# Performance work log

Hardware: AMD Instinct MI355X
Metric: run time of the kernel (lower is better)

Reference implementation:

```python
import jax, jax.numpy as jnp
import numpy as np

D_STATE = 48
D_CONV = 4
DT_RANK = 12
SEG = 4  # path=3 -> segment=2**(3-1)
EPS = 1e-5


def _layernorm(x, w, b):
    m = x.mean(-1, keepdims=True)
    v = x.var(-1, keepdims=True)
    return (x - m) / jnp.sqrt(v + EPS) * w + b


def _batchnorm(x, g, b):
    # x: (B, N, C); BatchNorm1d in train mode normalizes per channel over (B, N)
    m = x.mean(axis=(0, 1))
    v = x.var(axis=(0, 1))
    return (x - m) / jnp.sqrt(v + EPS) * g + b


def _selective_scan(u, delta, A, Bm, Cm):
    # u, delta: (b,l,d); A: (d,n); Bm, Cm: (b,l,n)
    def step(h, inp):
        dt_t, b_t, c_t, u_t = inp  # (b,d),(b,n),(b,n),(b,d)
        dA = jnp.exp(dt_t[:, :, None] * A)                  # (b,d,n)
        h = dA * h + (dt_t * u_t)[:, :, None] * b_t[:, None, :]
        y = jnp.einsum('bdn,bn->bd', h, c_t)
        return h, y
    b, l, d = u.shape
    n = A.shape[1]
    h0 = jnp.zeros((b, d, n), u.dtype)
    xs = (delta.transpose(1, 0, 2), Bm.transpose(1, 0, 2),
          Cm.transpose(1, 0, 2), u.transpose(1, 0, 2))
    _, ys = jax.lax.scan(step, h0, xs)
    return ys.transpose(1, 0, 2)


def _mamba(x, in_proj_w, conv_w, conv_b, x_proj_w, dt_proj_w, dt_proj_b,
           A_log, D_param, out_proj_w):
    b, l, _ = x.shape
    xz = x @ in_proj_w.T                                   # (b,l,2*di)
    xa, z = jnp.split(xz, 2, axis=-1)
    # causal depthwise conv1d, kernel D_CONV, left pad D_CONV-1
    xp = jnp.pad(xa, ((0, 0), (D_CONV - 1, 0), (0, 0)))
    xc = sum(xp[:, k:k + l, :] * conv_w[:, k] for k in range(D_CONV)) + conv_b
    xc = jax.nn.silu(xc)
    x_dbl = xc @ x_proj_w.T                                # (b,l,dt_rank+2n)
    dtl = x_dbl[..., :DT_RANK]
    Bm = x_dbl[..., DT_RANK:DT_RANK + D_STATE]
    Cm = x_dbl[..., DT_RANK + D_STATE:]
    dt = jax.nn.softplus(dtl @ dt_proj_w.T + dt_proj_b)
    A = -jnp.exp(A_log)
    y = _selective_scan(xc, dt, A, Bm, Cm) + xc * D_param
    y = y * jax.nn.silu(z)
    return y @ out_proj_w.T


def _ffn(x, fc1_w, bn1_g, bn1_b, r_w, i_w, rb, ib, fc2_w, bn2_g, bn2_b):
    h = jax.nn.relu(_batchnorm(x @ fc1_w.T, bn1_g, bn1_b))
    hf = jnp.fft.fft(h, axis=1, norm='ortho')
    # torch.einsum('bnc,cc->bnc', X, W) takes diag(W): elementwise channel scale
    rd = jnp.diagonal(r_w)
    idg = jnp.diagonal(i_w)
    real = jax.nn.relu(hf.real * rd - hf.imag * idg + rb)
    imag = jax.nn.relu(hf.imag * rd + hf.real * idg + ib)
    xt = jnp.fft.ifft(jax.lax.complex(real, imag), axis=1, norm='ortho').real
    return _batchnorm(xt @ fc2_w.T, bn2_g, bn2_b)


def _block(x, in_proj_w, conv_w, conv_b, x_proj_w, dt_proj_w, dt_proj_b,
           A_log, D_param, out_proj_w, mnorm_w, mnorm_b,
           norm1_w, norm1_b, norm2_w, norm2_b,
           fc1_w, bn1_g, bn1_b, r_w, i_w, rb, ib, fc2_w, bn2_g, bn2_b):
    B, D, C = x.shape
    tt = D // SEG
    # multi-path shifted copies: first D - i*tt positions shifted by i*tt,
    # tail keeps the original values (clone semantics)
    shifts = [x] + [jnp.concatenate([x[:, i * tt:], x[:, D - i * tt:]], axis=1)
                    for i in range(1, SEG)]
    xo = jnp.concatenate(shifts, axis=0)                   # (SEG*B, D, C)
    y = _mamba(_layernorm(xo, mnorm_w, mnorm_b),
               in_proj_w, conv_w, conv_b, x_proj_w, dt_proj_w, dt_proj_b,
               A_log, D_param, out_proj_w)
    ys = y.reshape(SEG, B, D, C)
    segs = [ys[0][:, :tt]]
    for i in range(1, SEG):
        s = ys[0][:, tt * i:tt * (i + 1)]
        for j in range(i):
            s = s + ys[j + 1][:, tt * (i - j - 1):tt * (i - j)]
        segs.append(s / (i + 1))
    xo0 = jnp.concatenate(segs, axis=1)                    # (B, D, C)
    x1 = x + _layernorm(xo0, norm1_w, norm1_b)
    x2 = x1 + _ffn(_layernorm(x1, norm2_w, norm2_b),
                   fc1_w, bn1_g, bn1_b, r_w, i_w, rb, ib, fc2_w, bn2_g, bn2_b)
    return x2


def setup_inputs() -> dict:
    key = jax.random.key(0)
    ks = jax.random.split(key, 16)
    s = 0.02
    B, L, C = 8, 512, 192
    DI, HD = 384, 384  # d_inner = 2*dim, ffn hidden = mlp_ratio*dim
    rn = lambda k, shp: jax.random.normal(k, shp, dtype=jnp.float32)
    return dict(
        x=rn(ks[0], (B, L, C)),
        in_proj_w=s * rn(ks[1], (2 * DI, C)),
        conv_w=s * rn(ks[2], (DI, D_CONV)),
        conv_b=s * rn(ks[3], (DI,)),
        x_proj_w=s * rn(ks[4], (DT_RANK + 2 * D_STATE, DI)),
        dt_proj_w=s * rn(ks[5], (DI, DT_RANK)),
        dt_proj_b=s * rn(ks[6], (DI,)),
        A_log=jnp.log(jnp.tile(jnp.arange(1, D_STATE + 1, dtype=jnp.float32), (DI, 1))),
        D_param=jnp.ones((DI,), jnp.float32),
        out_proj_w=s * rn(ks[7], (C, DI)),
        mnorm_w=jnp.ones((C,), jnp.float32), mnorm_b=jnp.zeros((C,), jnp.float32),
        norm1_w=jnp.ones((C,), jnp.float32), norm1_b=jnp.zeros((C,), jnp.float32),
        norm2_w=jnp.ones((C,), jnp.float32), norm2_b=jnp.zeros((C,), jnp.float32),
        fc1_w=s * rn(ks[8], (HD, C)),
        bn1_g=jnp.ones((HD,), jnp.float32), bn1_b=jnp.zeros((HD,), jnp.float32),
        r_w=s * rn(ks[9], (HD, HD)),
        i_w=s * rn(ks[10], (HD, HD)),
        rb=s * rn(ks[11], (HD,)),
        ib=s * rn(ks[12], (HD,)),
        fc2_w=s * rn(ks[13], (C, HD)),
        bn2_g=jnp.ones((C,), jnp.float32), bn2_b=jnp.zeros((C,), jnp.float32),
    )


def reference(x, in_proj_w, conv_w, conv_b, x_proj_w, dt_proj_w, dt_proj_b,
              A_log, D_param, out_proj_w, mnorm_w, mnorm_b,
              norm1_w, norm1_b, norm2_w, norm2_b,
              fc1_w, bn1_g, bn1_b, r_w, i_w, rb, ib, fc2_w, bn2_g, bn2_b):
    return _block(x, in_proj_w, conv_w, conv_b, x_proj_w, dt_proj_w, dt_proj_b,
                  A_log, D_param, out_proj_w, mnorm_w, mnorm_b,
                  norm1_w, norm1_b, norm2_w, norm2_b,
                  fc1_w, bn1_g, bn1_b, r_w, i_w, rb, ib, fc2_w, bn2_g, bn2_b)
```

## Files before the change

### kernel.cpp

```cpp
#include <hip/hip_runtime.h>
#include <math.h>

#define LSEQ 512
#define CDIM 192
#define DIN  384
#define NST  48
#define RNK  12
#define NBT  32
#define NB   8
#define NCH  16
#define LCH  32

static __device__ __forceinline__ float sigmoidf_(float x) { return 1.f / (1.f + __expf(-x)); }

typedef __attribute__((ext_vector_type(8))) short bshort8;
typedef __attribute__((ext_vector_type(4))) float f32x4;

static __device__ __forceinline__ short f2bf(float x) {
    unsigned u = __float_as_uint(x);
    unsigned r = (u + 0x7FFFu + ((u >> 16) & 1u)) >> 16;
    return (short)r;
}
static __device__ __forceinline__ float bfhi2f(unsigned pk) { return __uint_as_float(pk & 0xffff0000u); }
static __device__ __forceinline__ float bflo2f(unsigned pk) { return __uint_as_float(pk << 16); }

#define SP 40
template<int BM, int BN, int GATE>
__global__ __launch_bounds__(256) void gemm_mfma_kernel(
    const float* __restrict__ A, const float* __restrict__ B, float* __restrict__ C,
    int M, int N, int K, int lda, int ldb, int ldc,
    long long sA, long long sB_, long long sC_,
    int transB, int accsub,
    const float* __restrict__ gxc, const float* __restrict__ gxz, const float* __restrict__ gD)
{
    constexpr int WM = BM / 2, WN = BN / 2, MI = WM / 16, NI = WN / 16;
    __shared__ short As[BM * SP];
    __shared__ short Bs[BN * SP];
    int tid = threadIdx.x;
    int m0 = blockIdx.x * BM, n0 = blockIdx.y * BN;
    if (GATE) {
        int sseg = m0 >> 12, t0 = m0 & 511;
        if ((t0 >> 7) + sseg > 3) return;
    }
    A += (long long)blockIdx.z * sA;
    B += (long long)blockIdx.z * sB_;
    C += (long long)blockIdx.z * sC_;
    int lane = tid & 63, wid = tid >> 6;
    int wr = wid >> 1, wc = wid & 1;
    int lr = lane & 15, lg = lane >> 4;
    f32x4 acc[MI][NI] = {};

    for (int k0 = 0; k0 < K; k0 += 32) {
#pragma unroll
        for (int it = 0; it < BM * 8 / 256; ++it) {
            int idx = tid + it * 256;
            int row = idx >> 3, kq = idx & 7;
            long long gm = m0 + row;
            float4 v = *(const float4*)(A + gm * lda + k0 + kq * 4);
            if (GATE) {
                int sseg = (int)(gm >> 12), bb = (int)((gm >> 9) & 7), tt = (int)(gm & 511);
                long long src = (long long)bb * 512 + tt + 128 * sseg;
                float4 xcv = *(const float4*)(gxc + src * 384 + k0 + kq * 4);
                float4 zv  = *(const float4*)(gxz + src * 768 + 384 + k0 + kq * 4);
                float4 Dv  = *(const float4*)(gD + k0 + kq * 4);
                v.x = (v.x + xcv.x * Dv.x) * (zv.x * sigmoidf_(zv.x));
                v.y = (v.y + xcv.y * Dv.y) * (zv.y * sigmoidf_(zv.y));
                v.z = (v.z + xcv.z * Dv.z) * (zv.z * sigmoidf_(zv.z));
                v.w = (v.w + xcv.w * Dv.w) * (zv.w * sigmoidf_(zv.w));
            }
            short4 b4 = make_short4(f2bf(v.x), f2bf(v.y), f2bf(v.z), f2bf(v.w));
            *(short4*)(&As[row * SP + kq * 4]) = b4;
        }
        if (transB) {
#pragma unroll
            for (int it = 0; it < BN * 8 / 256; ++it) {
                int idx = tid + it * 256;
                int row = idx >> 3, kq = idx & 7;
                int gn = n0 + row;
                float4 v = make_float4(0.f, 0.f, 0.f, 0.f);
                if (gn < N) v = *(const float4*)(B + (long long)gn * ldb + k0 + kq * 4);
                short4 b4 = make_short4(f2bf(v.x), f2bf(v.y), f2bf(v.z), f2bf(v.w));
                *(short4*)(&Bs[row * SP + kq * 4]) = b4;
            }
        } else {
            constexpr int NQ = BN / 4;
#pragma unroll
            for (int it = 0; it < 32 * NQ / 256; ++it) {
                int idx = tid + it * 256;
                int k = idx / NQ, nq = idx % NQ;
                int gn = n0 + nq * 4;
                float4 v = make_float4(0.f, 0.f, 0.f, 0.f);
                if (gn < N) v = *(const float4*)(B + (long long)(k0 + k) * ldb + gn);
                Bs[(nq * 4 + 0) * SP + k] = f2bf(v.x);
                Bs[(nq * 4 + 1) * SP + k] = f2bf(v.y);
                Bs[(nq * 4 + 2) * SP + k] = f2bf(v.z);
                Bs[(nq * 4 + 3) * SP + k] = f2bf(v.w);
            }
        }
        __syncthreads();
        bshort8 af[MI], bfr[NI];
#pragma unroll
        for (int i = 0; i < MI; ++i)
            af[i] = *(const bshort8*)(&As[(wr * WM + i * 16 + lr) * SP + lg * 8]);
#pragma unroll
        for (int j = 0; j < NI; ++j)
            bfr[j] = *(const bshort8*)(&Bs[(wc * WN + j * 16 + lr) * SP + lg * 8]);
#pragma unroll
        for (int i = 0; i < MI; ++i)
#pragma unroll
            for (int j = 0; j < NI; ++j)
                acc[i][j] = __builtin_amdgcn_mfma_f32_16x16x32_bf16(af[i], bfr[j], acc[i][j], 0, 0, 0);
        __syncthreads();
    }
#pragma unroll
    for (int i = 0; i < MI; ++i) {
        int gm = m0 + wr * WM + i * 16 + lg * 4;
#pragma unroll
        for (int j = 0; j < NI; ++j) {
            int gn = n0 + wc * WN + j * 16 + lr;
            if (gn < N) {
#pragma unroll
                for (int r = 0; r < 4; ++r) {
                    long long idx = (long long)(gm + r) * ldc + gn;
                    float v = acc[i][j][r];
                    if (accsub) C[idx] = C[idx] - v;
                    else C[idx] = v;
                }
            }
        }
    }
}

__global__ __launch_bounds__(256) void dft_fwd_kernel(
    const short* __restrict__ Tc, const short* __restrict__ Ts,
    const float* __restrict__ Bm, float* __restrict__ C1, float* __restrict__ C2,
    const float* __restrict__ stats, const float* __restrict__ bng,
    const float* __restrict__ bnb, float invM)
{
    __shared__ short Acs[64 * SP];
    __shared__ short Ass[64 * SP];
    __shared__ short Bs[64 * SP];
    int tid = threadIdx.x;
    int m0 = blockIdx.x * 64, n0 = blockIdx.y * 64;
    const float* B = Bm + (long long)blockIdx.z * 196608;
    float* c1 = C1 + (long long)blockIdx.z * 122880;
    float* c2 = C2 + (long long)blockIdx.z * 122880;
    int lane = tid & 63, wid = tid >> 6;
    int wr = wid >> 1, wc = wid & 1;
    int lr = lane & 15, lg = lane >> 4;
    int nn = tid & 63, k8 = tid >> 6;
    int f = n0 + nn;
    float sc, sh;
    {
        float m = stats[f] * invM;
        float vv = stats[384 + f] * invM - m * m;
        sc = rsqrtf(vv + 1e-5f) * bng[f];
        sh = bnb[f] - m * sc;
    }
    f32x4 a1[2][2] = {}, a2[2][2] = {};
    for (int k0 = 0; k0 < 512; k0 += 32) {
        {
            *(uint4*)(&Acs[nn * SP + k8 * 8]) =
                *(const uint4*)(Tc + (long long)(m0 + nn) * 512 + k0 + k8 * 8);
            *(uint4*)(&Ass[nn * SP + k8 * 8]) =
                *(const uint4*)(Ts + (long long)(m0 + nn) * 512 + k0 + k8 * 8);
        }
        {
            bshort8 pk;
#pragma unroll
            for (int j = 0; j < 8; ++j) {
                float v = B[(long long)(k0 + k8 * 8 + j) * 384 + f];
                v = fmaxf(fmaf(v, sc, sh), 0.f);
                pk[j] = f2bf(v);
            }
            *(bshort8*)(&Bs[nn * SP + k8 * 8]) = pk;
        }
        __syncthreads();
        bshort8 af[2], sf[2], bf[2];
#pragma unroll
        for (int i = 0; i < 2; ++i) {
            af[i] = *(const bshort8*)(&Acs[(wr * 32 + i * 16 + lr) * SP + lg * 8]);
            sf[i] = *(const bshort8*)(&Ass[(wr * 32 + i * 16 + lr) * SP + lg * 8]);
            bf[i] = *(const bshort8*)(&Bs[(wc * 32 + i * 16 + lr) * SP + lg * 8]);
        }
#pragma unroll
        for (int i = 0; i < 2; ++i)
#pragma unroll
            for (int j = 0; j < 2; ++j) {
                a1[i][j] = __builtin_amdgcn_mfma_f32_16x16x32_bf16(af[i], bf[j], a1[i][j], 0, 0, 0);
                a2[i][j] = __builtin_amdgcn_mfma_f32_16x16x32_bf16(sf[i], bf[j], a2[i][j], 0, 0, 0);
            }
        __syncthreads();
    }
#pragma unroll
    for (int i = 0; i < 2; ++i) {
        int gm = m0 + wr * 32 + i * 16 + lg * 4;
#pragma unroll
        for (int j = 0; j < 2; ++j) {
            int gn = n0 + wc * 32 + j * 16 + lr;
#pragma unroll
            for (int r = 0; r < 4; ++r) {
                c1[(long long)(gm + r) * 384 + gn] = a1[i][j][r];
                c2[(long long)(gm + r) * 384 + gn] = a2[i][j][r];
            }
        }
    }
}

__global__ __launch_bounds__(256) void dft_inv_kernel(
    const short* __restrict__ Tc, const short* __restrict__ Ts,
    const float* __restrict__ Br, const float* __restrict__ Bi,
    float* __restrict__ Co,
    const float* __restrict__ rw, const float* __restrict__ iw,
    const float* __restrict__ rbv, const float* __restrict__ ibv)
{
    __shared__ short Acs[64 * SP];
    __shared__ short Ans[64 * SP];
    __shared__ short Brs[64 * SP];
    __shared__ short Bis[64 * SP];
    int tid = threadIdx.x;
    int m0 = blockIdx.x * 64, n0 = blockIdx.y * 64;
    const float* br = Br + (long long)blockIdx.z * 122880;
    const float* bi = Bi + (long long)blockIdx.z * 122880;
    float* co = Co + (long long)blockIdx.z * 196608;
    int lane = tid & 63, wid = tid >> 6;
    int wr = wid >> 1, wc = wid & 1;
    int lr = lane & 15, lg = lane >> 4;
    int nn = tid & 63, k8 = tid >> 6;
    int f = n0 + nn;
    float rd = rw[(long long)f * 384 + f];
    float id = iw[(long long)f * 384 + f];
    float rbs = rbv[f], ibs = ibv[f];
    f32x4 acc[2][2] = {};
    for (int k0 = 0; k0 < 288; k0 += 32) {
        {
            *(uint4*)(&Acs[nn * SP + k8 * 8]) =
                *(const uint4*)(Tc + (long long)(m0 + nn) * 512 + k0 + k8 * 8);
            uint4 ps = *(const uint4*)(Ts + (long long)(m0 + nn) * 512 + k0 + k8 * 8);
            ps.x ^= 0x80008000u; ps.y ^= 0x80008000u; ps.z ^= 0x80008000u; ps.w ^= 0x80008000u;
            *(uint4*)(&Ans[nn * SP + k8 * 8]) = ps;
        }
        {
            bshort8 pr, pi;
#pragma unroll
            for (int j = 0; j < 8; ++j) {
                int kg = k0 + k8 * 8 + j;
                short vr = 0, vi = 0;
                if (kg <= 256) {
                    float Re = br[(long long)kg * 384 + f];
                    float S  = bi[(long long)kg * 384 + f];
                    float wgt = (kg == 0 || kg == 256) ? 0.5f : 1.f;
                    float t1 = Re * rd + rbs, t2 = S * id;
                    float t3 = Re * id + ibs, t4 = S * rd;
                    float Rs = wgt * (fmaxf(t1 + t2, 0.f) + fmaxf(t1 - t2, 0.f));
                    float Is = wgt * (fmaxf(t3 - t4, 0.f) - fmaxf(t3 + t4, 0.f));
                    vr = f2bf(Rs);
                    vi = f2bf(Is);
                }
                pr[j] = vr;
                pi[j] = vi;
            }
            *(bshort8*)(&Brs[nn * SP + k8 * 8]) = pr;
            *(bshort8*)(&Bis[nn * SP + k8 * 8]) = pi;
        }
        __syncthreads();
        bshort8 af[2], nf[2], rf[2], iff[2];
#pragma unroll
        for (int i = 0; i < 2; ++i) {
            af[i]  = *(const bshort8*)(&Acs[(wr * 32 + i * 16 + lr) * SP + lg * 8]);
            nf[i]  = *(const bshort8*)(&Ans[(wr * 32 + i * 16 + lr) * SP + lg * 8]);
            rf[i]  = *(const bshort8*)(&Brs[(wc * 32 + i * 16 + lr) * SP + lg * 8]);
            iff[i] = *(const bshort8*)(&Bis[(wc * 32 + i * 16 + lr) * SP + lg * 8]);
        }
#pragma unroll
        for (int i = 0; i < 2; ++i)
#pragma unroll
            for (int j = 0; j < 2; ++j) {
                acc[i][j] = __builtin_amdgcn_mfma_f32_16x16x32_bf16(af[i], rf[j], acc[i][j], 0, 0, 0);
                acc[i][j] = __builtin_amdgcn_mfma_f32_16x16x32_bf16(nf[i], iff[j], acc[i][j], 0, 0, 0);
            }
        __syncthreads();
    }
#pragma unroll
    for (int i = 0; i < 2; ++i) {
        int gm = m0 + wr * 32 + i * 16 + lg * 4;
#pragma unroll
        for (int j = 0; j < 2; ++j) {
            int gn = n0 + wc * 32 + j * 16 + lr;
#pragma unroll
            for (int r = 0; r < 4; ++r)
                co[(long long)(gm + r) * 384 + gn] = acc[i][j][r];
        }
    }
}

__global__ __launch_bounds__(64) void ln_kernel(
    const float* __restrict__ in, const float* __restrict__ w, const float* __restrict__ b,
    float* __restrict__ out)
{
    int row = blockIdx.x;
    const float* xr = in + (long long)row * CDIM;
    int lane = threadIdx.x;
    float v0 = xr[lane], v1 = xr[lane + 64], v2 = xr[lane + 128];
    float s1 = v0 + v1 + v2;
    float s2 = v0 * v0 + v1 * v1 + v2 * v2;
#pragma unroll
    for (int off = 32; off >= 1; off >>= 1) {
        s1 += __shfl_xor(s1, off);
        s2 += __shfl_xor(s2, off);
    }
    float mean = s1 * (1.f / 192.f);
    float var = s2 * (1.f / 192.f) - mean * mean;
    float rstd = rsqrtf(var + 1e-5f);
    float* orow = out + (long long)row * CDIM;
    orow[lane]       = (v0 - mean) * rstd * w[lane] + b[lane];
    orow[lane + 64]  = (v1 - mean) * rstd * w[lane + 64] + b[lane + 64];
    orow[lane + 128] = (v2 - mean) * rstd * w[lane + 128] + b[lane + 128];
}

__global__ __launch_bounds__(256) void conv_silu_kernel(
    const float* __restrict__ xz, const float* __restrict__ cw,
    const float* __restrict__ cb, float* __restrict__ xc)
{
    long long idx = (long long)blockIdx.x * 256 + threadIdx.x;
    int d = (int)(idx % DIN);
    long long rt = idx / DIN;
    int t = (int)(rt & 511);
    long long base = rt - t;
    float acc = cb[d];
#pragma unroll
    for (int k = 0; k < 4; ++k) {
        int tt = t + k - 3;
        if (tt >= 0) acc = fmaf(xz[(base + tt) * 768 + d], cw[d * 4 + k], acc);
    }
    xc[idx] = acc * sigmoidf_(acc);
}

__global__ __launch_bounds__(256) void scan_pass1(
    const float* __restrict__ xdbl0, const float* __restrict__ xc0,
    const float* __restrict__ dt_w, const float* __restrict__ dt_b,
    const float* __restrict__ A_log, float* __restrict__ ylocal,
    float* __restrict__ hpart, float* __restrict__ sumdt, float* __restrict__ cumdtg)
{
    int d0 = blockIdx.x * 32, bb = blockIdx.y, c = blockIdx.z;
    __shared__ float sBC[LCH][96];
    __shared__ unsigned sdd[LCH][32];
    __shared__ float sdtl[LCH][12];
    __shared__ float sdtw[32][12];
    __shared__ float sdtb[32];
    int tid = threadIdx.x;
    int p = tid >> 3, q = tid & 7, d = d0 + p;
    for (int i = tid; i < 384; i += 256) sdtw[i / 12][i % 12] = dt_w[(d0 + i / 12) * 12 + i % 12];
    if (tid < 32) sdtb[tid] = dt_b[d0 + tid];
    float A0 = -__expf(A_log[d * NST + 6 * q]);
    float Ad = -__expf(A_log[d * NST + 6 * q + 1]) - A0;
    long long srcbase = (long long)bb * LSEQ + c * LCH;
    for (int i = tid; i < LCH * 108; i += 256) {
        int tt = i / 108, cc = i % 108;
        float v = xdbl0[(srcbase + tt) * 108 + cc];
        if (cc < 12) sdtl[tt][cc] = v;
        else if (cc < 60) { int n = cc - 12; int qq = (n * 43) >> 8; sBC[tt][qq * 12 + (n - qq * 6)] = v; }
        else              { int n = cc - 60; int qq = (n * 43) >> 8; sBC[tt][qq * 12 + 6 + (n - qq * 6)] = v; }
    }
    __syncthreads();
    for (int i = tid; i < LCH * 32; i += 256) {
        int tt = i >> 5, j = i & 31;
        float s = sdtb[j];
#pragma unroll
        for (int r = 0; r < 12; ++r) s = fmaf(sdtl[tt][r], sdtw[j][r], s);
        s = fmaxf(s, 0.f) + log1pf(__expf(-fabsf(s)));
        float u = xc0[(srcbase + tt) * DIN + d0 + j];
        unsigned hi = (unsigned)(unsigned short)f2bf(s);
        unsigned lo = (unsigned)(unsigned short)f2bf(s * u);
        sdd[tt][j] = (hi << 16) | lo;
    }
    __syncthreads();
    float h0r = 0.f, h1r = 0.f, h2r = 0.f, h3r = 0.f, h4r = 0.f, h5r = 0.f;
    float cum = 0.f;
    long long locbase = ((long long)(bb * NCH + c)) * LCH;
#pragma unroll 2
    for (int tt = 0; tt < LCH; ++tt) {
        unsigned pk = sdd[tt][p];
        float s = bfhi2f(pk), du = bflo2f(pk);
        cum += s;
        float f = __expf(s * A0);
        float w = __expf(s * Ad);
        float4 v0 = *(const float4*)&sBC[tt][q * 12];
        float4 v1 = *(const float4*)&sBC[tt][q * 12 + 4];
        float4 v2 = *(const float4*)&sBC[tt][q * 12 + 8];
        float y;
        h0r = fmaf(f, h0r, du * v0.x); y = h0r * v1.z;          f *= w;
        h1r = fmaf(f, h1r, du * v0.y); y = fmaf(h1r, v1.w, y);  f *= w;
        h2r = fmaf(f, h2r, du * v0.z); y = fmaf(h2r, v2.x, y);  f *= w;
        h3r = fmaf(f, h3r, du * v0.w); y = fmaf(h3r, v2.y, y);  f *= w;
        h4r = fmaf(f, h4r, du * v1.x); y = fmaf(h4r, v2.z, y);  f *= w;
        h5r = fmaf(f, h5r, du * v1.y); y = fmaf(h5r, v2.w, y);
        y += __shfl_xor(y, 1);
        y += __shfl_xor(y, 2);
        y += __shfl_xor(y, 4);
        if (q == 0) {
            ylocal[(locbase + tt) * DIN + d] = y;
            cumdtg[(srcbase + tt) * DIN + d] = cum;
        }
    }
    if (q == 0) sumdt[((long long)(bb * NCH + c)) * DIN + d] = cum;
    float* hp = &hpart[(((long long)(bb * NCH + c)) * DIN + d) * NST + 6 * q];
    hp[0] = h0r; hp[1] = h1r; hp[2] = h2r; hp[3] = h3r; hp[4] = h4r; hp[5] = h5r;
}

__global__ __launch_bounds__(256) void scan_pass2(
    const float* __restrict__ A_log, const float* __restrict__ sumdt,
    const float* __restrict__ hpart, float* __restrict__ hinbuf)
{
    long long idx = (long long)blockIdx.x * 256 + threadIdx.x;
    if (idx >= 8LL * DIN * NST) return;
    int n = (int)(idx % NST);
    long long rem = idx / NST;
    int d = (int)(rem % DIN);
    int bb = (int)(rem / DIN);
    float An = -__expf(A_log[d * NST + n]);
    float S[NCH], P[NCH];
#pragma unroll
    for (int c = 0; c < NCH; ++c) {
        S[c] = hpart[(((long long)(bb * NCH + c)) * DIN + d) * NST + n];
        P[c] = __expf(An * sumdt[((long long)(bb * NCH + c)) * DIN + d]);
    }
#pragma unroll
    for (int s = 0; s < 4; ++s) {
        float hin = 0.f;
#pragma unroll
        for (int c = 0; c < NCH; ++c) {
            if (c < 4 * s) continue;
            int ch = c - 4 * s;
            hinbuf[(((long long)(bb * 64 + s * 16 + ch)) * DIN + d) * NST + n] = hin;
            hin = fmaf(P[c], hin, S[c]);
        }
    }
}

#define TT3 16
__global__ __launch_bounds__(256) void scan_pass3(
    const float* __restrict__ xdbl0, const float* __restrict__ cumdtg,
    const float* __restrict__ A_log, const float* __restrict__ hin_g,
    const float* __restrict__ ylocal, float* __restrict__ yout)
{
    int c = blockIdx.z >> 1, tq = blockIdx.z & 1;
    int toff = tq * TT3;
    int d0 = blockIdx.x * 32, bb = blockIdx.y;
    int smax = (c >> 2) < 3 ? (c >> 2) : 3;
    __shared__ float sC[TT3][64];
    __shared__ float scum[TT3][32];
    int tid = threadIdx.x;
    int p = tid >> 3, q = tid & 7, d = d0 + p;
    float A0 = -__expf(A_log[d * NST + 6 * q]);
    float Ad = -__expf(A_log[d * NST + 6 * q + 1]) - A0;
    float g0[6] = {}, g1[6] = {}, g2[6] = {}, g3[6] = {};
    {
        const float* hp0 = &hin_g[(((long long)(bb * 64 + 0 * 16 + c)) * DIN + d) * NST + 6 * q];
#pragma unroll
        for (int k = 0; k < 6; ++k) g0[k] = hp0[k];
        if (smax >= 1) {
            const float* hp1 = &hin_g[(((long long)(bb * 64 + 1 * 16 + (c - 4))) * DIN + d) * NST + 6 * q];
#pragma unroll
            for (int k = 0; k < 6; ++k) g1[k] = hp1[k];
        }
        if (smax >= 2) {
            const float* hp2 = &hin_g[(((long long)(bb * 64 + 2 * 16 + (c - 8))) * DIN + d) * NST + 6 * q];
#pragma unroll
            for (int k = 0; k < 6; ++k) g2[k] = hp2[k];
        }
        if (smax >= 3) {
            const float* hp3 = &hin_g[(((long long)(bb * 64 + 3 * 16 + (c - 12))) * DIN + d) * NST + 6 * q];
#pragma unroll
            for (int k = 0; k < 6; ++k) g3[k] = hp3[k];
        }
    }
    long long srcbase = (long long)bb * LSEQ + c * LCH + toff;
    long long locbase = ((long long)(bb * NCH + c)) * LCH + toff;
    long long ob0 = ((long long)(0 * NB + bb)) * LSEQ + (long long)c * LCH + toff;
    long long ob1 = ((long long)(1 * NB + bb)) * LSEQ + (long long)(c - 4) * LCH + toff;
    long long ob2 = ((long long)(2 * NB + bb)) * LSEQ + (long long)(c - 8) * LCH + toff;
    long long ob3 = ((long long)(3 * NB + bb)) * LSEQ + (long long)(c - 12) * LCH + toff;
    for (int i = tid; i < TT3 * 48; i += 256) {
        int tt = i / 48, n = i % 48;
        int qq = (n * 43) >> 8;
        sC[tt][qq * 8 + n - qq * 6] = xdbl0[(srcbase + tt) * 108 + 60 + n];
    }
    for (int i = tid; i < TT3 * 32; i += 256) {
        int tt = i >> 5, j = i & 31;
        scum[tt][j] = cumdtg[(srcbase + tt) * DIN + d0 + j];
    }
    __syncthreads();
#pragma unroll 2
    for (int tt = 0; tt < TT3; ++tt) {
        float cd = scum[tt][p];
        float f = __expf(cd * A0);
        float w = __expf(cd * Ad);
        float4 c03 = *(const float4*)&sC[tt][q * 8];
        float4 c45 = *(const float4*)&sC[tt][q * 8 + 4];
        float Cf0 = c03.x * f; f *= w;
        float Cf1 = c03.y * f; f *= w;
        float Cf2 = c03.z * f; f *= w;
        float Cf3 = c03.w * f; f *= w;
        float Cf4 = c45.x * f; f *= w;
        float Cf5 = c45.y * f;
        float a0 = Cf0 * g0[0];
        a0 = fmaf(Cf1, g0[1], a0); a0 = fmaf(Cf2, g0[2], a0);
        a0 = fmaf(Cf3, g0[3], a0); a0 = fmaf(Cf4, g0[4], a0);
        a0 = fmaf(Cf5, g0[5], a0);
        a0 += __shfl_xor(a0, 1); a0 += __shfl_xor(a0, 2); a0 += __shfl_xor(a0, 4);
        float a1 = 0.f, a2 = 0.f, a3 = 0.f;
        if (smax >= 1) {
            a1 = Cf0 * g1[0];
            a1 = fmaf(Cf1, g1[1], a1); a1 = fmaf(Cf2, g1[2], a1);
            a1 = fmaf(Cf3, g1[3], a1); a1 = fmaf(Cf4, g1[4], a1);
            a1 = fmaf(Cf5, g1[5], a1);
            a1 += __shfl_xor(a1, 1); a1 += __shfl_xor(a1, 2); a1 += __shfl_xor(a1, 4);
        }
        if (smax >= 2) {
            a2 = Cf0 * g2[0];
            a2 = fmaf(Cf1, g2[1], a2); a2 = fmaf(Cf2, g2[2], a2);
            a2 = fmaf(Cf3, g2[3], a2); a2 = fmaf(Cf4, g2[4], a2);
            a2 = fmaf(Cf5, g2[5], a2);
            a2 += __shfl_xor(a2, 1); a2 += __shfl_xor(a2, 2); a2 += __shfl_xor(a2, 4);
        }
        if (smax >= 3) {
            a3 = Cf0 * g3[0];
            a3 = fmaf(Cf1, g3[1], a3); a3 = fmaf(Cf2, g3[2], a3);
            a3 = fmaf(Cf3, g3[3], a3); a3 = fmaf(Cf4, g3[4], a3);
            a3 = fmaf(Cf5, g3[5], a3);
            a3 += __shfl_xor(a3, 1); a3 += __shfl_xor(a3, 2); a3 += __shfl_xor(a3, 4);
        }
        if (q == 0) {
            float yl = ylocal[(locbase + tt) * DIN + d];
            yout[(ob0 + tt) * DIN + d] = yl + a0;
            if (smax >= 1) yout[(ob1 + tt) * DIN + d] = yl + a1;
            if (smax >= 2) yout[(ob2 + tt) * DIN + d] = yl + a2;
            if (smax >= 3) yout[(ob3 + tt) * DIN + d] = yl + a3;
        }
    }
}

__global__ __launch_bounds__(64) void combine_ln_kernel(
    const float* __restrict__ ym, const float* __restrict__ x,
    const float* __restrict__ w, const float* __restrict__ b,
    const float* __restrict__ w2, const float* __restrict__ b2,
    float* __restrict__ x1, float* __restrict__ lnx1)
{
    int row = blockIdx.x;
    int t = row & 511, bb = row >> 9;
    int i = t >> 7;
    int lane = threadIdx.x;
    float vals[3];
#pragma unroll
    for (int cp = 0; cp < 3; ++cp) {
        int c = lane + cp * 64;
        float v = ym[((long long)bb * LSEQ + t) * CDIM + c];
        for (int j = 1; j <= i; ++j)
            v += ym[((long long)(j * NB + bb) * LSEQ + (t - 128 * j)) * CDIM + c];
        vals[cp] = v / (float)(i + 1);
    }
    float s1 = vals[0] + vals[1] + vals[2];
    float s2 = vals[0] * vals[0] + vals[1] * vals[1] + vals[2] * vals[2];
#pragma unroll
    for (int off = 32; off >= 1; off >>= 1) {
        s1 += __shfl_xor(s1, off);
        s2 += __shfl_xor(s2, off);
    }
    float mean = s1 * (1.f / 192.f);
    float var = s2 * (1.f / 192.f) - mean * mean;
    float rstd = rsqrtf(var + 1e-5f);
    long long base = (long long)row * CDIM;
    float xv[3];
#pragma unroll
    for (int cp = 0; cp < 3; ++cp) {
        int c = lane + cp * 64;
        xv[cp] = x[base + c] + (vals[cp] - mean) * rstd * w[c] + b[c];
        x1[base + c] = xv[cp];
    }
    float t1 = xv[0] + xv[1] + xv[2];
    float t2 = xv[0] * xv[0] + xv[1] * xv[1] + xv[2] * xv[2];
#pragma unroll
    for (int off = 32; off >= 1; off >>= 1) {
        t1 += __shfl_xor(t1, off);
        t2 += __shfl_xor(t2, off);
    }
    float mean2 = t1 * (1.f / 192.f);
    float var2 = t2 * (1.f / 192.f) - mean2 * mean2;
    float rstd2 = rsqrtf(var2 + 1e-5f);
#pragma unroll
    for (int cp = 0; cp < 3; ++cp) {
        int c = lane + cp * 64;
        lnx1[base + c] = (xv[cp] - mean2) * rstd2 * w2[c] + b2[c];
    }
}

__global__ __launch_bounds__(256) void bnstats_kernel(
    const float* __restrict__ X, float* __restrict__ stats, int NF)
{
    int fl = threadIdx.x & 63;
    int f = blockIdx.x * 64 + fl;
    int r = threadIdx.x >> 6;
    int t0 = blockIdx.y * 128;
    float s1 = 0.f, s2 = 0.f;
    for (int i = 0; i < 32; ++i) {
        int row = t0 + r * 32 + i;
        float v = X[(long long)row * NF + f];
        s1 += v;
        s2 += v * v;
    }
    __shared__ float p1[4][64], p2[4][64];
    p1[r][fl] = s1;
    p2[r][fl] = s2;
    __syncthreads();
    if (threadIdx.x < 64) {
        int ff = blockIdx.x * 64 + threadIdx.x;
        float a = p1[0][threadIdx.x] + p1[1][threadIdx.x] + p1[2][threadIdx.x] + p1[3][threadIdx.x];
        float c = p2[0][threadIdx.x] + p2[1][threadIdx.x] + p2[2][threadIdx.x] + p2[3][threadIdx.x];
        atomicAdd(&stats[ff], a);
        atomicAdd(&stats[NF + ff], c);
    }
}

__global__ __launch_bounds__(256) void bnapply_kernel(
    const float* __restrict__ X, const float* __restrict__ stats,
    const float* __restrict__ g, const float* __restrict__ b,
    const float* __restrict__ residual, float* __restrict__ out,
    int NF, int relu, float invM)
{
    long long idx = (long long)blockIdx.x * 256 + threadIdx.x;
    int f = (int)(idx % NF);
    float mean = stats[f] * invM;
    float var = stats[NF + f] * invM - mean * mean;
    float v = (X[idx] - mean) * rsqrtf(var + 1e-5f) * g[f] + b[f];
    if (relu) v = fmaxf(v, 0.f);
    if (residual) v += residual[idx];
    out[idx] = v;
}

__global__ __launch_bounds__(256) void dft_table_kernel(short* __restrict__ tc, short* __restrict__ ts)
{
    int idx = blockIdx.x * 256 + threadIdx.x;
    int k = idx >> 9, t = idx & 511;
    int r = (k * t) & 511;
    float th = (float)r * (6.283185307179586f / 512.f);
    float s, c;
    __sincosf(th, &s, &c);
    const float inv = 0.04419417382415922f;
    tc[idx] = f2bf(c * inv);
    ts[idx] = f2bf(s * inv);
}

extern "C" void kernel_launch(void* const* d_in, const int* in_sizes, int n_in,
                              void* d_out, int out_size, void* d_ws, size_t ws_size,
                              hipStream_t stream)
{
    const float* x        = (const float*)d_in[0];
    const float* in_w     = (const float*)d_in[1];
    const float* conv_w   = (const float*)d_in[2];
    const float* conv_b   = (const float*)d_in[3];
    const float* xproj_w  = (const float*)d_in[4];
    const float* dtp_w    = (const float*)d_in[5];
    const float* dtp_b    = (const float*)d_in[6];
    const float* A_log    = (const float*)d_in[7];
    const float* D_par    = (const float*)d_in[8];
    const float* outp_w   = (const float*)d_in[9];
    const float* mnw      = (const float*)d_in[10];
    const float* mnb      = (const float*)d_in[11];
    const float* n1w      = (const float*)d_in[12];
    const float* n1b      = (const float*)d_in[13];
    const float* n2w      = (const float*)d_in[14];
    const float* n2b      = (const float*)d_in[15];
    const float* fc1_w    = (const float*)d_in[16];
    const float* bn1g     = (const float*)d_in[17];
    const float* bn1b     = (const float*)d_in[18];
    const float* r_w      = (const float*)d_in[19];
    const float* i_w      = (const float*)d_in[20];
    const float* rb       = (const float*)d_in[21];
    const float* ib       = (const float*)d_in[22];
    const float* fc2_w    = (const float*)d_in[23];
    const float* bn2g     = (const float*)d_in[24];
    const float* bn2b     = (const float*)d_in[25];
    float* out = (float*)d_out;
    float* ws = (float*)d_ws;

    float* lnx0   = ws;
    float* xz0    = lnx0   + 786432LL;
    float* xc0    = xz0    + 3145728LL;
    float* xdbl0  = xc0    + 1572864LL;
    float* yscan  = xdbl0  + 442368LL;
    float* hinb   = yscan  + 6291456LL;
    float* cumdtg = hinb   + 9437184LL;
    float* hpart  = cumdtg + 1572864LL;
    float* ylocal = hpart  + 2359296LL;
    float* sumdt  = ylocal + 1572864LL;
    float* ymout = hinb;
    float* x1    = lnx0;
    float* lnx1  = yscan;
    float* hbuf  = yscan + 786432LL;
    float* hfr   = yscan + 2359296LL;
    float* hfi   = yscan + 3342336LL;
    float* xt    = xz0;
    float* g0    = xz0 + 1572864LL;
    short* tabc_bf = (short*)xc0;
    short* tabs_bf = (short*)(xc0 + 131072LL);
    float* stats = xc0 + 262144LL;

    ln_kernel<<<dim3(NB * LSEQ), dim3(64), 0, stream>>>(x, mnw, mnb, lnx0);

    gemm_mfma_kernel<64, 128, 0><<<dim3(64, 6, 1), dim3(256), 0, stream>>>(
        lnx0, in_w, xz0, 4096, 768, 192, 192, 192, 768, 0, 0, 0, 1, 0,
        nullptr, nullptr, nullptr);

    conv_silu_kernel<<<dim3(6144), dim3(256), 0, stream>>>(xz0, conv_w, conv_b, xc0);

    gemm_mfma_kernel<64, 64, 0><<<dim3(64, 2, 1), dim3(256), 0, stream>>>(
        xc0, xproj_w, xdbl0, 4096, 108, 384, 384, 384, 108, 0, 0, 0, 1, 0,
        nullptr, nullptr, nullptr);

    scan_pass1<<<dim3(12, 8, NCH), dim3(256), 0, stream>>>(
        xdbl0, xc0, dtp_w, dtp_b, A_log, ylocal, hpart, sumdt, cumdtg);
    scan_pass2<<<dim3(576), dim3(256), 0, stream>>>(A_log, sumdt, hpart, hinb);
    scan_pass3<<<dim3(12, 8, NCH * 2), dim3(256), 0, stream>>>(
        xdbl0, cumdtg, A_log, hinb, ylocal, yscan);

    gemm_mfma_kernel<64, 64, 1><<<dim3(256, 3, 1), dim3(256), 0, stream>>>(
        yscan, outp_w, ymout, 16384, 192, 384, 384, 384, 192, 0, 0, 0, 1, 0,
        xc0, xz0, D_par);

    hipMemsetAsync(stats, 0, 2048 * sizeof(float), stream);

    combine_ln_kernel<<<dim3(NB * LSEQ), dim3(64), 0, stream>>>(
        ymout, x, n1w, n1b, n2w, n2b, x1, lnx1);

    gemm_mfma_kernel<64, 64, 0><<<dim3(64, 6, 1), dim3(256), 0, stream>>>(
        lnx1, fc1_w, hbuf, 4096, 384, 192, 192, 192, 384, 0, 0, 0, 1, 0,
        nullptr, nullptr, nullptr);

    bnstats_kernel<<<dim3(6, 32), dim3(256), 0, stream>>>(hbuf, stats, 384);

    dft_table_kernel<<<dim3(1024), dim3(256), 0, stream>>>(tabc_bf, tabs_bf);

    dft_fwd_kernel<<<dim3(5, 6, 8), dim3(256), 0, stream>>>(
        tabc_bf, tabs_bf, hbuf, hfr, hfi, stats, bn1g, bn1b, 1.f / 4096.f);

    dft_inv_kernel<<<dim3(8, 6, 8), dim3(256), 0, stream>>>(
        tabc_bf, tabs_bf, hfr, hfi, xt, r_w, i_w, rb, ib);

    gemm_mfma_kernel<32, 64, 0><<<dim3(128, 3, 1), dim3(256), 0, stream>>>(
        xt, fc2_w, g0, 4096, 192, 384, 384, 384, 192, 0, 0, 0, 1, 0,
        nullptr, nullptr, nullptr);

    bnstats_kernel<<<dim3(3, 32), dim3(256), 0, stream>>>(g0, stats + 1024, 192);
    bnapply_kernel<<<dim3(3072), dim3(256), 0, stream>>>(
        g0, stats + 1024, bn2g, bn2b, x1, out, 192, 0, 1.f / 4096.f);
}
```

Baseline: 260.4 us.

## Collapse four segment scans into one averaged carried-state scan before out-projection

The four shifted-segment Mamba outputs are now averaged before the out-projection rather than after it. This relies on the linearity of out_proj and of the gating applied to y. scan_pass2 builds a single weighted-average incoming state per chunk (hbar), so scan_pass3 computes one correction instead of up to four and updates ylocal in place. The out-projection GEMM runs on 4096 rows instead of 16384, and combine_ln no longer sums four segment outputs. Workspace aliases are reshuffled to fit the smaller buffers; the in-place ylocal update and the new hfi placement risk aliasing errors.

```diff
diff --git a/kernel.cpp b/kernel.cpp
--- a/kernel.cpp
+++ b/kernel.cpp
@@ -6,7 +6,6 @@
 #define DIN  384
 #define NST  48
 #define RNK  12
-#define NBT  32
 #define NB   8
 #define NCH  16
 #define LCH  32
@@ -38,10 +37,6 @@
     __shared__ short Bs[BN * SP];
     int tid = threadIdx.x;
     int m0 = blockIdx.x * BM, n0 = blockIdx.y * BN;
-    if (GATE) {
-        int sseg = m0 >> 12, t0 = m0 & 511;
-        if ((t0 >> 7) + sseg > 3) return;
-    }
     A += (long long)blockIdx.z * sA;
     B += (long long)blockIdx.z * sB_;
     C += (long long)blockIdx.z * sC_;
@@ -58,10 +53,8 @@
             long long gm = m0 + row;
             float4 v = *(const float4*)(A + gm * lda + k0 + kq * 4);
             if (GATE) {
-                int sseg = (int)(gm >> 12), bb = (int)((gm >> 9) & 7), tt = (int)(gm & 511);
-                long long src = (long long)bb * 512 + tt + 128 * sseg;
-                float4 xcv = *(const float4*)(gxc + src * 384 + k0 + kq * 4);
-                float4 zv  = *(const float4*)(gxz + src * 768 + 384 + k0 + kq * 4);
+                float4 xcv = *(const float4*)(gxc + gm * 384 + k0 + kq * 4);
+                float4 zv  = *(const float4*)(gxz + gm * 768 + 384 + k0 + kq * 4);
                 float4 Dv  = *(const float4*)(gD + k0 + kq * 4);
                 v.x = (v.x + xcv.x * Dv.x) * (zv.x * sigmoidf_(zv.x));
                 v.y = (v.y + xcv.y * Dv.y) * (zv.y * sigmoidf_(zv.y));
@@ -377,7 +370,6 @@
     __syncthreads();
     float h0r = 0.f, h1r = 0.f, h2r = 0.f, h3r = 0.f, h4r = 0.f, h5r = 0.f;
     float cum = 0.f;
-    long long locbase = ((long long)(bb * NCH + c)) * LCH;
 #pragma unroll 2
     for (int tt = 0; tt < LCH; ++tt) {
         unsigned pk = sdd[tt][p];
@@ -399,7 +391,7 @@
         y += __shfl_xor(y, 2);
         y += __shfl_xor(y, 4);
         if (q == 0) {
-            ylocal[(locbase + tt) * DIN + d] = y;
+            ylocal[(srcbase + tt) * DIN + d] = y;
             cumdtg[(srcbase + tt) * DIN + d] = cum;
         }
     }
@@ -410,7 +402,7 @@
 
 __global__ __launch_bounds__(256) void scan_pass2(
     const float* __restrict__ A_log, const float* __restrict__ sumdt,
-    const float* __restrict__ hpart, float* __restrict__ hinbuf)
+    const float* __restrict__ hpart, float* __restrict__ hbarb)
 {
     long long idx = (long long)blockIdx.x * 256 + threadIdx.x;
     if (idx >= 8LL * DIN * NST) return;
@@ -419,68 +411,39 @@
     int d = (int)(rem % DIN);
     int bb = (int)(rem / DIN);
     float An = -__expf(A_log[d * NST + n]);
-    float S[NCH], P[NCH];
+    float G = 0.f;
 #pragma unroll
     for (int c = 0; c < NCH; ++c) {
-        S[c] = hpart[(((long long)(bb * NCH + c)) * DIN + d) * NST + n];
-        P[c] = __expf(An * sumdt[((long long)(bb * NCH + c)) * DIN + d]);
-    }
-#pragma unroll
-    for (int s = 0; s < 4; ++s) {
-        float hin = 0.f;
-#pragma unroll
-        for (int c = 0; c < NCH; ++c) {
-            if (c < 4 * s) continue;
-            int ch = c - 4 * s;
-            hinbuf[(((long long)(bb * 64 + s * 16 + ch)) * DIN + d) * NST + n] = hin;
-            hin = fmaf(P[c], hin, S[c]);
-        }
+        float nc = (float)((c >> 2) + 1);
+        hbarb[(((long long)(bb * NCH + c)) * DIN + d) * NST + n] = G / nc;
+        float S = hpart[(((long long)(bb * NCH + c)) * DIN + d) * NST + n];
+        float P = __expf(An * sumdt[((long long)(bb * NCH + c)) * DIN + d]);
+        G = fmaf(P, G, nc * S);
     }
 }
 
 #define TT3 16
 __global__ __launch_bounds__(256) void scan_pass3(
     const float* __restrict__ xdbl0, const float* __restrict__ cumdtg,
-    const float* __restrict__ A_log, const float* __restrict__ hin_g,
-    const float* __restrict__ ylocal, float* __restrict__ yout)
+    const float* __restrict__ A_log, const float* __restrict__ hbarb,
+    float* __restrict__ ylocal)
 {
     int c = blockIdx.z >> 1, tq = blockIdx.z & 1;
     int toff = tq * TT3;
     int d0 = blockIdx.x * 32, bb = blockIdx.y;
-    int smax = (c >> 2) < 3 ? (c >> 2) : 3;
     __shared__ float sC[TT3][64];
     __shared__ float scum[TT3][32];
     int tid = threadIdx.x;
     int p = tid >> 3, q = tid & 7, d = d0 + p;
     float A0 = -__expf(A_log[d * NST + 6 * q]);
     float Ad = -__expf(A_log[d * NST + 6 * q + 1]) - A0;
-    float g0[6] = {}, g1[6] = {}, g2[6] = {}, g3[6] = {};
+    float g0[6];
     {
-        const float* hp0 = &hin_g[(((long long)(bb * 64 + 0 * 16 + c)) * DIN + d) * NST + 6 * q];
+        const float* hp0 = &hbarb[(((long long)(bb * NCH + c)) * DIN + d) * NST + 6 * q];
 #pragma unroll
         for (int k = 0; k < 6; ++k) g0[k] = hp0[k];
-        if (smax >= 1) {
-            const float* hp1 = &hin_g[(((long long)(bb * 64 + 1 * 16 + (c - 4))) * DIN + d) * NST + 6 * q];
-#pragma unroll
-            for (int k = 0; k < 6; ++k) g1[k] = hp1[k];
-        }
-        if (smax >= 2) {
-            const float* hp2 = &hin_g[(((long long)(bb * 64 + 2 * 16 + (c - 8))) * DIN + d) * NST + 6 * q];
-#pragma unroll
-            for (int k = 0; k < 6; ++k) g2[k] = hp2[k];
-        }
-        if (smax >= 3) {
-            const float* hp3 = &hin_g[(((long long)(bb * 64 + 3 * 16 + (c - 12))) * DIN + d) * NST + 6 * q];
-#pragma unroll
-            for (int k = 0; k < 6; ++k) g3[k] = hp3[k];
-        }
     }
     long long srcbase = (long long)bb * LSEQ + c * LCH + toff;
-    long long locbase = ((long long)(bb * NCH + c)) * LCH + toff;
-    long long ob0 = ((long long)(0 * NB + bb)) * LSEQ + (long long)c * LCH + toff;
-    long long ob1 = ((long long)(1 * NB + bb)) * LSEQ + (long long)(c - 4) * LCH + toff;
-    long long ob2 = ((long long)(2 * NB + bb)) * LSEQ + (long long)(c - 8) * LCH + toff;
-    long long ob3 = ((long long)(3 * NB + bb)) * LSEQ + (long long)(c - 12) * LCH + toff;
     for (int i = tid; i < TT3 * 48; i += 256) {
         int tt = i / 48, n = i % 48;
         int qq = (n * 43) >> 8;
@@ -498,45 +461,17 @@
         float w = __expf(cd * Ad);
         float4 c03 = *(const float4*)&sC[tt][q * 8];
         float4 c45 = *(const float4*)&sC[tt][q * 8 + 4];
-        float Cf0 = c03.x * f; f *= w;
-        float Cf1 = c03.y * f; f *= w;
-        float Cf2 = c03.z * f; f *= w;
-        float Cf3 = c03.w * f; f *= w;
-        float Cf4 = c45.x * f; f *= w;
-        float Cf5 = c45.y * f;
-        float a0 = Cf0 * g0[0];
-        a0 = fmaf(Cf1, g0[1], a0); a0 = fmaf(Cf2, g0[2], a0);
-        a0 = fmaf(Cf3, g0[3], a0); a0 = fmaf(Cf4, g0[4], a0);
-        a0 = fmaf(Cf5, g0[5], a0);
+        float a0;
+        a0 = c03.x * g0[0] * f;            f *= w;
+        a0 = fmaf(c03.y * g0[1], f, a0);   f *= w;
+        a0 = fmaf(c03.z * g0[2], f, a0);   f *= w;
+        a0 = fmaf(c03.w * g0[3], f, a0);   f *= w;
+        a0 = fmaf(c45.x * g0[4], f, a0);   f *= w;
+        a0 = fmaf(c45.y * g0[5], f, a0);
         a0 += __shfl_xor(a0, 1); a0 += __shfl_xor(a0, 2); a0 += __shfl_xor(a0, 4);
-        float a1 = 0.f, a2 = 0.f, a3 = 0.f;
-        if (smax >= 1) {
-            a1 = Cf0 * g1[0];
-            a1 = fmaf(Cf1, g1[1], a1); a1 = fmaf(Cf2, g1[2], a1);
-            a1 = fmaf(Cf3, g1[3], a1); a1 = fmaf(Cf4, g1[4], a1);
-            a1 = fmaf(Cf5, g1[5], a1);
-            a1 += __shfl_xor(a1, 1); a1 += __shfl_xor(a1, 2); a1 += __shfl_xor(a1, 4);
-        }
-        if (smax >= 2) {
-            a2 = Cf0 * g2[0];
-            a2 = fmaf(Cf1, g2[1], a2); a2 = fmaf(Cf2, g2[2], a2);
-            a2 = fmaf(Cf3, g2[3], a2); a2 = fmaf(Cf4, g2[4], a2);
-            a2 = fmaf(Cf5, g2[5], a2);
-            a2 += __shfl_xor(a2, 1); a2 += __shfl_xor(a2, 2); a2 += __shfl_xor(a2, 4);
-        }
-        if (smax >= 3) {
-            a3 = Cf0 * g3[0];
-            a3 = fmaf(Cf1, g3[1], a3); a3 = fmaf(Cf2, g3[2], a3);
-            a3 = fmaf(Cf3, g3[3], a3); a3 = fmaf(Cf4, g3[4], a3);
-            a3 = fmaf(Cf5, g3[5], a3);
-            a3 += __shfl_xor(a3, 1); a3 += __shfl_xor(a3, 2); a3 += __shfl_xor(a3, 4);
-        }
         if (q == 0) {
-            float yl = ylocal[(locbase + tt) * DIN + d];
-            yout[(ob0 + tt) * DIN + d] = yl + a0;
-            if (smax >= 1) yout[(ob1 + tt) * DIN + d] = yl + a1;
-            if (smax >= 2) yout[(ob2 + tt) * DIN + d] = yl + a2;
-            if (smax >= 3) yout[(ob3 + tt) * DIN + d] = yl + a3;
+            long long yi = (srcbase + tt) * DIN + d;
+            ylocal[yi] = ylocal[yi] + a0;
         }
     }
 }
@@ -548,18 +483,11 @@
     float* __restrict__ x1, float* __restrict__ lnx1)
 {
     int row = blockIdx.x;
-    int t = row & 511, bb = row >> 9;
-    int i = t >> 7;
     int lane = threadIdx.x;
+    long long base = (long long)row * CDIM;
     float vals[3];
 #pragma unroll
-    for (int cp = 0; cp < 3; ++cp) {
-        int c = lane + cp * 64;
-        float v = ym[((long long)bb * LSEQ + t) * CDIM + c];
-        for (int j = 1; j <= i; ++j)
-            v += ym[((long long)(j * NB + bb) * LSEQ + (t - 128 * j)) * CDIM + c];
-        vals[cp] = v / (float)(i + 1);
-    }
+    for (int cp = 0; cp < 3; ++cp) vals[cp] = ym[base + lane + cp * 64];
     float s1 = vals[0] + vals[1] + vals[2];
     float s2 = vals[0] * vals[0] + vals[1] * vals[1] + vals[2] * vals[2];
 #pragma unroll
@@ -570,7 +498,6 @@
     float mean = s1 * (1.f / 192.f);
     float var = s2 * (1.f / 192.f) - mean * mean;
     float rstd = rsqrtf(var + 1e-5f);
-    long long base = (long long)row * CDIM;
     float xv[3];
 #pragma unroll
     for (int cp = 0; cp < 3; ++cp) {
@@ -688,23 +615,23 @@
     float* xz0    = lnx0   + 786432LL;
     float* xc0    = xz0    + 3145728LL;
     float* xdbl0  = xc0    + 1572864LL;
-    float* yscan  = xdbl0  + 442368LL;
-    float* hinb   = yscan  + 6291456LL;
-    float* cumdtg = hinb   + 9437184LL;
+    float* ylocal = xdbl0  + 442368LL;
+    float* hbarb  = ylocal + 1572864LL;
+    float* cumdtg = hbarb  + 2359296LL;
     float* hpart  = cumdtg + 1572864LL;
-    float* ylocal = hpart  + 2359296LL;
-    float* sumdt  = ylocal + 1572864LL;
-    float* ymout = hinb;
+    float* sumdt  = hpart  + 2359296LL;
+    float* ymout = hbarb;
     float* x1    = lnx0;
-    float* lnx1  = yscan;
-    float* hbuf  = yscan + 786432LL;
-    float* hfr   = yscan + 2359296LL;
-    float* hfi   = yscan + 3342336LL;
-    float* xt    = xz0;
-    float* g0    = xz0 + 1572864LL;
+    float* lnx1  = cumdtg;
+    float* hbuf  = xz0;
+    float* hfr   = xz0 + 1572864LL;
+    float* hfi   = xz0 + 2555904LL;
+    float* xt    = ylocal;
+    float* g0    = hpart;
     short* tabc_bf = (short*)xc0;
     short* tabs_bf = (short*)(xc0 + 131072LL);
     float* stats = xc0 + 262144LL;
+    hfi = xc0 + 270336LL;
 
     ln_kernel<<<dim3(NB * LSEQ), dim3(64), 0, stream>>>(x, mnw, mnb, lnx0);
 
@@ -720,12 +647,12 @@
 
     scan_pass1<<<dim3(12, 8, NCH), dim3(256), 0, stream>>>(
         xdbl0, xc0, dtp_w, dtp_b, A_log, ylocal, hpart, sumdt, cumdtg);
-    scan_pass2<<<dim3(576), dim3(256), 0, stream>>>(A_log, sumdt, hpart, hinb);
+    scan_pass2<<<dim3(576), dim3(256), 0, stream>>>(A_log, sumdt, hpart, hbarb);
     scan_pass3<<<dim3(12, 8, NCH * 2), dim3(256), 0, stream>>>(
-        xdbl0, cumdtg, A_log, hinb, ylocal, yscan);
-
-    gemm_mfma_kernel<64, 64, 1><<<dim3(256, 3, 1), dim3(256), 0, stream>>>(
-        yscan, outp_w, ymout, 16384, 192, 384, 384, 384, 192, 0, 0, 0, 1, 0,
+        xdbl0, cumdtg, A_log, hbarb, ylocal);
+
+    gemm_mfma_kernel<32, 64, 1><<<dim3(128, 3, 1), dim3(256), 0, stream>>>(
+        ylocal, outp_w, ymout, 4096, 192, 384, 384, 384, 192, 0, 0, 0, 1, 0,
         xc0, xz0, D_par);
 
     hipMemsetAsync(stats, 0, 2048 * sizeof(float), stream);
```

Measured after the change: 231.4 us. 1.13x faster.
